# Kernel optimization log

Measured on AMD Instinct MI355X. Metric: run time of the kernel, lower is better.

Reference implementation:

```python
import jax, jax.numpy as jnp
import numpy as np

N = 50000
E = 800000
H = 96
NUM_IN = 11
PE_DIM = 24
NUM_OUT = 1
NUM_LAYERS = 4
NUM_GRAPHS = 256


def _linear_params(key, d_in, d_out):
    k1, k2 = jax.random.split(key)
    bound = 1.0 / np.sqrt(d_in)
    w = jax.random.uniform(k1, (d_in, d_out), jnp.float32, -bound, bound)
    b = jax.random.uniform(k2, (d_out,), jnp.float32, -bound, bound)
    return w, b


def setup_inputs() -> dict:
    key = jax.random.key(0)
    ks = jax.random.split(key, 32)
    x = jax.random.normal(ks[0], (N, NUM_IN), jnp.float32)
    pos = jax.random.normal(ks[1], (N, 3), jnp.float32)
    pe = jax.random.normal(ks[2], (N, PE_DIM), jnp.float32)
    edge_index = jax.random.randint(ks[3], (2, E), 0, N, jnp.int64)
    batch = jnp.sort(jax.random.randint(ks[4], (N,), 0, NUM_GRAPHS, jnp.int64))
    embed_w1, embed_b1 = _linear_params(ks[5], NUM_IN + PE_DIM, H)
    embed_w2, embed_b2 = _linear_params(ks[6], H, H)
    # per-layer stacked params
    msg_w1 = []; msg_b1 = []; msg_w2 = []; msg_b2 = []
    upd_w1 = []; upd_b1 = []; upd_w2 = []; upd_b2 = []
    for l in range(NUM_LAYERS):
        w, b = _linear_params(ks[7 + l], 2 * H + 1, H); msg_w1.append(w); msg_b1.append(b)
        w, b = _linear_params(ks[11 + l], H, H); msg_w2.append(w); msg_b2.append(b)
        w, b = _linear_params(ks[15 + l], 2 * H, H); upd_w1.append(w); upd_b1.append(b)
        w, b = _linear_params(ks[19 + l], H, H); upd_w2.append(w); upd_b2.append(b)
    pre_w1, pre_b1 = _linear_params(ks[23], H, H)
    pre_w2, pre_b2 = _linear_params(ks[24], H, H)
    ro_w1, ro_b1 = _linear_params(ks[25], H, H)
    ro_w2, ro_b2 = _linear_params(ks[26], H, NUM_OUT)
    return {
        'x': x, 'pos': pos, 'pe': pe, 'edge_index': edge_index, 'batch': batch,
        'embed_w1': embed_w1, 'embed_b1': embed_b1, 'embed_w2': embed_w2, 'embed_b2': embed_b2,
        'msg_w1': jnp.stack(msg_w1), 'msg_b1': jnp.stack(msg_b1),
        'msg_w2': jnp.stack(msg_w2), 'msg_b2': jnp.stack(msg_b2),
        'upd_w1': jnp.stack(upd_w1), 'upd_b1': jnp.stack(upd_b1),
        'upd_w2': jnp.stack(upd_w2), 'upd_b2': jnp.stack(upd_b2),
        'pre_w1': pre_w1, 'pre_b1': pre_b1, 'pre_w2': pre_w2, 'pre_b2': pre_b2,
        'ro_w1': ro_w1, 'ro_b1': ro_b1, 'ro_w2': ro_w2, 'ro_b2': ro_b2,
    }


def _egnn_forward(x, pos, pe, edge_index, batch,
                  embed_w1, embed_b1, embed_w2, embed_b2,
                  msg_w1, msg_b1, msg_w2, msg_b2,
                  upd_w1, upd_b1, upd_w2, upd_b2,
                  pre_w1, pre_b1, pre_w2, pre_b2,
                  ro_w1, ro_b1, ro_w2, ro_b2):
    silu = jax.nn.silu
    send, rec = edge_index[0], edge_index[1]
    h = jnp.concatenate([x, pe], axis=-1)
    h = silu(h @ embed_w1 + embed_b1) @ embed_w2 + embed_b2  # [N,H]
    dist = jnp.linalg.norm(pos[send] - pos[rec], axis=1)[:, None]  # [E,1]
    for l in range(NUM_LAYERS):
        state = jnp.concatenate([h[send], h[rec], dist], axis=1)  # [E,2H+1]
        msg = silu(silu(state @ msg_w1[l] + msg_b1[l]) @ msg_w2[l] + msg_b2[l])  # [E,H]
        aggr = jax.ops.segment_sum(msg, rec, num_segments=h.shape[0])  # [N,H]
        upd_in = jnp.concatenate([h, aggr], axis=1)
        update = silu(upd_in @ upd_w1[l] + upd_b1[l]) @ upd_w2[l] + upd_b2[l]
        h = h + update
    h = silu(h @ pre_w1 + pre_b1) @ pre_w2 + pre_b2
    pooled = jax.ops.segment_sum(h, batch, num_segments=NUM_GRAPHS)  # [G,H]
    out = silu(pooled @ ro_w1 + ro_b1) @ ro_w2 + ro_b2  # [G,1]
    return jnp.squeeze(out)


def reference(x, pos, pe, edge_index, batch,
              embed_w1, embed_b1, embed_w2, embed_b2,
              msg_w1, msg_b1, msg_w2, msg_b2,
              upd_w1, upd_b1, upd_w2, upd_b2,
              pre_w1, pre_b1, pre_w2, pre_b2,
              ro_w1, ro_b1, ro_w2, ro_b2):
    return _egnn_forward(x, pos, pe, edge_index, batch,
                         embed_w1, embed_b1, embed_w2, embed_b2,
                         msg_w1, msg_b1, msg_w2, msg_b2,
                         upd_w1, upd_b1, upd_w2, upd_b2,
                         pre_w1, pre_b1, pre_w2, pre_b2,
                         ro_w1, ro_b1, ro_w2, ro_b2)
```

## Files before the change

### kernel.cpp

```cpp
#include <hip/hip_runtime.h>
#include <hip/hip_bf16.h>

#define HDIM 96
#define TILE 128
#define NTILE 64

typedef __attribute__((ext_vector_type(8))) short  short8;
typedef __attribute__((ext_vector_type(4))) short  short4v;
typedef __attribute__((ext_vector_type(4))) float  float4v;
typedef __attribute__((ext_vector_type(2))) float  float2v;
typedef __attribute__((ext_vector_type(4))) unsigned int uint4v;
typedef __attribute__((ext_vector_type(2))) unsigned int uint2v;

static __device__ __forceinline__ short f2bf(float f){
    unsigned u = __float_as_uint(f);
    return (short)((u + 0x8000u) >> 16);
}
static __device__ __forceinline__ float bf2f(short s){
    unsigned u = ((unsigned)(unsigned short)s) << 16;
    return __uint_as_float(u);
}
static __device__ __forceinline__ float silu_f(float v){
    return v * __builtin_amdgcn_rcpf(1.0f + __expf(-v));
}
static __device__ __forceinline__ unsigned silu2_pack(float2v v){
    float e0 = __expf(-v[0]);
    float e1 = __expf(-v[1]);
    float2v ep = {e0, e1};
    const float2v one2 = {1.0f, 1.0f};
    ep += one2;
    float2v q = { __builtin_amdgcn_rcpf(ep[0]), __builtin_amdgcn_rcpf(ep[1]) };
    float2v res = v * q;
    unsigned pa = __float_as_uint(res[0]) + 0x8000u;
    unsigned pb = __float_as_uint(res[1]) + 0x8000u;
    return __builtin_amdgcn_perm(pb, pa, 0x07060302);
}

struct SwJob { const float* src; int ck; int ks; int ksrc; };
struct SwTable { SwJob j[22]; };

__global__ __launch_bounds__(256) void swizzle_all(SwTable T, const float* __restrict__ msg_w1,
                                                   short* __restrict__ dst, short* __restrict__ dst2,
                                                   int total1, int total2){
    int gid = blockIdx.x*256 + threadIdx.x;
    if (gid < total1) {
        int ksg = gid / 3072;
        int e   = gid % 3072;
        const float* src = T.j[0].src; int k0 = 0, ksrc = 0;
        #pragma unroll
        for (int jj = 0; jj < 22; ++jj){
            int s = T.j[jj].ck;
            if (ksg >= s && ksg < s + T.j[jj].ks){ src = T.j[jj].src; k0 = (ksg - s)*32; ksrc = T.j[jj].ksrc; }
        }
        int nt   = e >> 9;
        int rem  = e & 511;
        int lane = rem >> 3;
        int jx   = rem & 7;
        int k = k0 + ((lane >> 4) << 3) + jx;
        int f = nt*16 + (lane & 15);
        float v = (k < ksrc) ? src[(size_t)k*HDIM + f] : 0.0f;
        dst[gid] = f2bf(v);
    } else if (gid < total1 + total2) {
        int g2 = gid - total1;
        int layer = g2 / 18432;
        int e     = g2 % 18432;
        int ksg = e / 6144;
        int rem = e % 6144;
        int nt   = rem >> 9;
        int r2   = rem & 511;
        int lane = r2 >> 3;
        int jx   = r2 & 7;
        int k = ksg*32 + ((lane >> 4) << 3) + jx;
        int f = nt*16 + (lane & 15);
        int row = (f < 96) ? k : (96 + k);
        int col = (f < 96) ? f : (f - 96);
        dst2[g2] = f2bf(msg_w1[(size_t)layer*193*96 + (size_t)row*96 + col]);
    }
}

__global__ __launch_bounds__(256) void hist_kernel(const int* __restrict__ rec, int* __restrict__ deg, int E){
    int e = blockIdx.x*256 + threadIdx.x;
    if (e < E) atomicAdd(&deg[rec[e]], 1);
}

__global__ __launch_bounds__(256) void scan_part(const int* __restrict__ deg, int* __restrict__ part, int N){
    __shared__ int red[256];
    const int t = threadIdx.x;
    int base = blockIdx.x*1024;
    int s = 0;
    #pragma unroll
    for (int j=0;j<4;j++){ int i = base + j*256 + t; s += (i<N)?deg[i]:0; }
    red[t]=s; __syncthreads();
    #pragma unroll
    for (int off=128; off>0; off>>=1){ if (t<off) red[t]+=red[t+off]; __syncthreads(); }
    if (t==0) part[blockIdx.x]=red[0];
}
__global__ __launch_bounds__(256) void scan_top(int* __restrict__ part, int nb){
    __shared__ int buf[256];
    const int t = threadIdx.x;
    int v = (t < nb) ? part[t] : 0;
    buf[t] = v;
    __syncthreads();
    #pragma unroll
    for (int off=1; off<256; off<<=1){
        int u = (t>=off)?buf[t-off]:0;
        __syncthreads();
        buf[t] += u;
        __syncthreads();
    }
    if (t < nb) part[t] = buf[t] - v;
}
__global__ __launch_bounds__(256) void scan_final(const int* __restrict__ deg, const int* __restrict__ part,
                                                  int* __restrict__ cur, int N){
    __shared__ int tsum[256];
    const int t = threadIdx.x;
    int i0 = blockIdx.x*1024 + t*4;
    int a0 = (i0+0<N)?deg[i0+0]:0;
    int a1 = (i0+1<N)?deg[i0+1]:0;
    int a2 = (i0+2<N)?deg[i0+2]:0;
    int a3 = (i0+3<N)?deg[i0+3]:0;
    int s = a0+a1+a2+a3;
    tsum[t]=s; __syncthreads();
    #pragma unroll
    for (int off=1; off<256; off<<=1){
        int u = (t>=off)?tsum[t-off]:0;
        __syncthreads();
        tsum[t]+=u;
        __syncthreads();
    }
    int excl = tsum[t]-s + part[blockIdx.x];
    if (i0+0<N) cur[i0+0]=excl;
    if (i0+1<N) cur[i0+1]=excl+a0;
    if (i0+2<N) cur[i0+2]=excl+a0+a1;
    if (i0+3<N) cur[i0+3]=excl+a0+a1+a2;
}

__global__ __launch_bounds__(256) void scatter_kernel(
    const int* __restrict__ send, const int* __restrict__ rec, const float* __restrict__ pos,
    int* __restrict__ cur, int2* __restrict__ sd_s, int* __restrict__ rec_s, int E)
{
    int e = blockIdx.x*256 + threadIdx.x;
    if (e >= E) return;
    int s = send[e], r = rec[e];
    int p = atomicAdd(&cur[r], 1);
    float dx = pos[3*s]   - pos[3*r];
    float dy = pos[3*s+1] - pos[3*r+1];
    float dz = pos[3*s+2] - pos[3*r+2];
    float d = sqrtf(dx*dx + dy*dy + dz*dz);
    sd_s[p] = make_int2(s, __float_as_int(d));
    rec_s[p] = r;
}

__global__ __launch_bounds__(256,5) void edge_kernel(
    const short* __restrict__ SR,
    const int2* __restrict__ sd_s, const int* __restrict__ rec_s,
    const float* __restrict__ w1r192,
    const short* __restrict__ w2sw, const float* __restrict__ b2,
    float* __restrict__ aggr, float* __restrict__ stageA, float* __restrict__ stageB, int E)
{
    __shared__ short msgS[TILE*104];
    __shared__ int   recS[TILE];
    __shared__ int   startIdxS[TILE+1];
    __shared__ int   wcntS[2];
    const int t  = threadIdx.x;
    const int e0 = blockIdx.x * TILE;
    const int lane = t & 63;
    const int wv   = t >> 6;
    const int e_lo = wv * 32;
    const int col  = lane & 15;
    const int quad = lane >> 4;
    const int frow = quad * 4;
    const float4v fzero = {0.f,0.f,0.f,0.f};

    int se[2], re[2]; float dd[2];
    #pragma unroll
    for (int et=0; et<2; ++et){
        int ec = e0 + e_lo + et*16 + col; if (ec >= E) ec = E - 1;
        int2 sd = sd_s[ec];
        se[et] = sd.x; dd[et] = __int_as_float(sd.y);
        re[et] = rec_s[ec];
    }
    uint4v Svu[2][3], Rvu[2][3];
    #pragma unroll
    for (int et=0; et<2; ++et)
      #pragma unroll
      for (int ks=0; ks<3; ++ks){
        int f0 = ks*32 + quad*8;
        Svu[et][ks] = *(const uint4v*)(SR + (size_t)se[et]*192 + f0);
        Rvu[et][ks] = *(const uint4v*)(SR + (size_t)re[et]*192 + 96 + f0);
      }

    int myRec = 0;
    bool flag = false;
    if (t < TILE) {
        int e = e0 + t; if (e >= E) e = E - 1;
        myRec = rec_s[e];
        recS[t] = myRec;
        int ep = e0 + t - 1; if (ep >= E) ep = E - 1;
        flag = (t == 0) || (myRec != rec_s[ep]);
    }
    unsigned long long bmask = __ballot(flag ? 1 : 0);
    int pre = __popcll(bmask & ((1ull << (t & 63)) - 1ull));
    if (t < TILE && (t & 63) == 0) wcntS[t >> 6] = __popcll(bmask);

    const bool firstB = (e0 > 0) && (rec_s[e0-1] == rec_s[e0]);
    const bool lastB  = (e0 + TILE < E) && (rec_s[e0 + TILE] == rec_s[(e0+TILE-1 < E)? e0+TILE-1 : E-1]);

    __syncthreads();

    if (flag) startIdxS[pre + ((t >> 6) ? wcntS[0] : 0)] = t;
    if (t == 0) startIdxS[wcntS[0] + wcntS[1]] = TILE;

    short8 frag[2][3];
    #pragma unroll
    for (int et=0; et<2; ++et){
        float2v d2 = {dd[et], dd[et]};
        #pragma unroll
        for (int ks=0; ks<3; ++ks){
            int f0 = ks*32 + quad*8;
            float4v wa = *(const float4v*)(w1r192 + f0);
            float4v wb = *(const float4v*)(w1r192 + f0 + 4);
            uint4v su = Svu[et][ks], ru = Rvu[et][ks];
            uint4v fo;
            #pragma unroll
            for (int p=0;p<4;p++){
                float2v w2;
                if      (p==0) w2 = (float2v){wa[0], wa[1]};
                else if (p==1) w2 = (float2v){wa[2], wa[3]};
                else if (p==2) w2 = (float2v){wb[0], wb[1]};
                else           w2 = (float2v){wb[2], wb[3]};
                unsigned us = su[p], ur = ru[p];
                float2v s2 = { __uint_as_float(us << 16), __uint_as_float(us & 0xffff0000u) };
                float2v r2 = { __uint_as_float(ur << 16), __uint_as_float(ur & 0xffff0000u) };
                float2v v = s2 + r2 + d2*w2;
                fo[p] = silu2_pack(v);
            }
            short8 fr;
            __builtin_memcpy(&fr, &fo, 16);
            frag[et][ks] = fr;
        }
    }

    float4v acc2[2][6];
    #pragma unroll
    for (int i=0;i<2;i++)
      #pragma unroll
      for (int n=0;n<6;n++) acc2[i][n] = fzero;

    const short8* w2f = (const short8*)w2sw;
    #pragma unroll
    for (int ks = 0; ks < 3; ++ks) {
        #pragma unroll
        for (int mt = 0; mt < 6; ++mt) {
            short8 a = w2f[(ks*6+mt)*64 + lane];
            acc2[0][mt] = __builtin_amdgcn_mfma_f32_16x16x32_bf16(a, frag[0][ks], acc2[0][mt], 0, 0, 0);
            acc2[1][mt] = __builtin_amdgcn_mfma_f32_16x16x32_bf16(a, frag[1][ks], acc2[1][mt], 0, 0, 0);
        }
    }
    float4v b2v[6];
    #pragma unroll
    for (int mt=0; mt<6; ++mt) b2v[mt] = *(const float4v*)(b2 + mt*16 + frow);

    #pragma unroll
    for (int et=0; et<2; ++et){
        int e = e_lo + et*16 + col;
        bool valid = (e0 + e) < E;
        #pragma unroll
        for (int mt=0; mt<6; ++mt){
            float2v vlo = { acc2[et][mt][0] + b2v[mt][0], acc2[et][mt][1] + b2v[mt][1] };
            float2v vhi = { acc2[et][mt][2] + b2v[mt][2], acc2[et][mt][3] + b2v[mt][3] };
            unsigned ulo = silu2_pack(vlo);
            unsigned uhi = silu2_pack(vhi);
            if (!valid){ ulo = 0u; uhi = 0u; }
            uint2v st = {ulo, uhi};
            *(uint2v*)(msgS + e*104 + mt*16 + frow) = st;
        }
    }
    __syncthreads();

    const int nseg = wcntS[0] + wcntS[1];
    const int items = nseg * 12;
    for (int item = t; item < items; item += 256){
        int s  = item / 12;
        int fg = item - s*12;
        int r0 = startIdxS[s], r1 = startIdxS[s+1];
        float2v s01 = {0.f,0.f}, s23 = {0.f,0.f}, s45 = {0.f,0.f}, s67 = {0.f,0.f};
        for (int r = r0; r < r1; ++r){
            const unsigned* pp = (const unsigned*)(msgS + r*104 + fg*8);
            unsigned p0 = pp[0], p1 = pp[1], p2 = pp[2], p3 = pp[3];
            float2v a0 = { __uint_as_float(p0 << 16), __uint_as_float(p0 & 0xffff0000u) };
            float2v a1 = { __uint_as_float(p1 << 16), __uint_as_float(p1 & 0xffff0000u) };
            float2v a2 = { __uint_as_float(p2 << 16), __uint_as_float(p2 & 0xffff0000u) };
            float2v a3 = { __uint_as_float(p3 << 16), __uint_as_float(p3 & 0xffff0000u) };
            s01 += a0; s23 += a1; s45 += a2; s67 += a3;
        }
        int node = recS[r0];
        float* dstp;
        if (s == 0 && firstB)            dstp = stageB + (size_t)node*HDIM + fg*8;
        else if (s == nseg-1 && lastB)   dstp = stageA + (size_t)node*HDIM + fg*8;
        else                             dstp = aggr   + (size_t)node*HDIM + fg*8;
        float4v lo = {s01[0], s01[1], s23[0], s23[1]};
        float4v hi = {s45[0], s45[1], s67[0], s67[1]};
        *(float4v*)(dstp)     = lo;
        *(float4v*)(dstp + 4) = hi;
    }
}

__global__ __launch_bounds__(256,3) void update_kernel(
    short* __restrict__ hbf, const float* __restrict__ aggr,
    const float* __restrict__ stageA, const float* __restrict__ stageB,
    const int* __restrict__ deg, const int* __restrict__ cur,
    const short* __restrict__ w1sw, const float* __restrict__ b1,
    const short* __restrict__ w2sw, const float* __restrict__ b2,
    const short* __restrict__ w1sr_next, const float* __restrict__ msgb1_next,
    short* __restrict__ SR,
    const short* __restrict__ pw1, const float* __restrict__ pb1,
    const short* __restrict__ pw2, const float* __restrict__ pb2,
    const int* __restrict__ batch, float* __restrict__ pooled, int N)
{
    __shared__ short stateS[NTILE*208];
    __shared__ int   batchS[NTILE];
    __shared__ int   startIdxS[NTILE+1];
    __shared__ int   nsegS;
    const int t  = threadIdx.x;
    const int n0 = blockIdx.x * NTILE;

    #pragma unroll
    for (int it = 0; it < 6; ++it) {
        int q = it*256 + t;
        int c = q % 24;
        int i = q / 24;
        int node = n0 + i;
        if (c < 12) {
            uint4v v = {0u,0u,0u,0u};
            if (node < N) v = *(const uint4v*)(hbf + (size_t)node*HDIM + c*8);
            *(uint4v*)(stateS + i*200 + c*8) = v;
        } else {
            int cc = c - 12;
            short8 s8 = {0,0,0,0,0,0,0,0};
            if (node < N) {
                int dg = deg[node];
                int en = cur[node];
                int st = en - dg;
                bool bnd = (dg > 0) && (st/TILE != (en-1)/TILE);
                float4v a0, a1;
                if (bnd) {
                    size_t b = (size_t)node*HDIM + cc*8;
                    a0 = *(const float4v*)(stageA + b)     + *(const float4v*)(stageB + b);
                    a1 = *(const float4v*)(stageA + b + 4) + *(const float4v*)(stageB + b + 4);
                } else {
                    a0 = *(const float4v*)(aggr + (size_t)node*HDIM + cc*8);
                    a1 = *(const float4v*)(aggr + (size_t)node*HDIM + cc*8 + 4);
                }
                s8[0]=f2bf(a0[0]); s8[1]=f2bf(a0[1]); s8[2]=f2bf(a0[2]); s8[3]=f2bf(a0[3]);
                s8[4]=f2bf(a1[0]); s8[5]=f2bf(a1[1]); s8[6]=f2bf(a1[2]); s8[7]=f2bf(a1[3]);
            }
            *(short8*)(stateS + i*200 + HDIM + cc*8) = s8;
        }
    }
    __syncthreads();

    const int lane = t & 63;
    const int wv   = t >> 6;
    const int rb   = wv * 16;
    const int col  = lane & 15;
    const int quad = lane >> 4;
    const int koff = quad * 8;
    const int frow = quad * 4;
    const float4v fzero = {0.f,0.f,0.f,0.f};

    float4v acc[6];
    #pragma unroll
    for (int n=0;n<6;n++) acc[n] = fzero;

    const short8* w1f = (const short8*)w1sw;
    #pragma unroll
    for (int ks = 0; ks < 6; ++ks) {
        short8 bb = *(const short8*)(stateS + (rb+col)*200 + ks*32 + koff);
        #pragma unroll
        for (int mt = 0; mt < 6; ++mt) {
            short8 a = w1f[(ks*6+mt)*64 + lane];
            acc[mt] = __builtin_amdgcn_mfma_f32_16x16x32_bf16(a, bb, acc[mt], 0, 0, 0);
        }
    }
    float4v b1v[6];
    #pragma unroll
    for (int mt=0; mt<6; ++mt) b1v[mt] = *(const float4v*)(b1 + mt*16 + frow);
    __syncthreads();

    short* t1S = stateS;
    {
        int e = rb + col;
        #pragma unroll
        for (int mt=0; mt<6; ++mt){
            short4v sv;
            #pragma unroll
            for (int r=0;r<4;r++) sv[r] = f2bf(silu_f(acc[mt][r] + b1v[mt][r]));
            *(short4v*)(t1S + e*104 + mt*16 + frow) = sv;
        }
    }
    __syncthreads();

    float4v acc2[6];
    #pragma unroll
    for (int n=0;n<6;n++) acc2[n] = fzero;

    const short8* w2f = (const short8*)w2sw;
    #pragma unroll
    for (int ks = 0; ks < 3; ++ks) {
        short8 bb = *(const short8*)(t1S + (rb+col)*104 + ks*32 + koff);
        #pragma unroll
        for (int mt = 0; mt < 6; ++mt) {
            short8 a = w2f[(ks*6+mt)*64 + lane];
            acc2[mt] = __builtin_amdgcn_mfma_f32_16x16x32_bf16(a, bb, acc2[mt], 0, 0, 0);
        }
    }
    float4v b2v[6];
    #pragma unroll
    for (int mt=0; mt<6; ++mt) b2v[mt] = *(const float4v*)(b2 + mt*16 + frow);
    __syncthreads();

    {
        int erow = rb + col;
        int node = n0 + erow;
        bool valid = node < N;
        size_t base = (size_t)node*HDIM;
        #pragma unroll
        for (int mt=0; mt<6; ++mt){
            int f0 = mt*16 + frow;
            short4v ov = {0,0,0,0};
            if (valid) ov = *(const short4v*)(hbf + base + f0);
            float4v o;
            #pragma unroll
            for (int r=0;r<4;r++) o[r] = bf2f(ov[r]) + acc2[mt][r] + b2v[mt][r];
            short4v sv = {f2bf(o[0]), f2bf(o[1]), f2bf(o[2]), f2bf(o[3])};
            if (valid) *(short4v*)(hbf + base + f0) = sv;
            *(short4v*)(stateS + erow*104 + f0) = sv;
        }
    }

    if (w1sr_next) {
        __syncthreads();
        float4v accS[12];
        #pragma unroll
        for (int n=0;n<12;n++) accS[n] = fzero;

        const short8* wsf = (const short8*)w1sr_next;
        #pragma unroll
        for (int ks = 0; ks < 3; ++ks) {
            short8 bb = *(const short8*)(stateS + (rb+col)*104 + ks*32 + koff);
            #pragma unroll
            for (int mt = 0; mt < 12; ++mt) {
                short8 a = wsf[(ks*12+mt)*64 + lane];
                accS[mt] = __builtin_amdgcn_mfma_f32_16x16x32_bf16(a, bb, accS[mt], 0, 0, 0);
            }
        }
        float4v bnv[6];
        #pragma unroll
        for (int mt=0; mt<6; ++mt) bnv[mt] = *(const float4v*)(msgb1_next + mt*16 + frow);

        {
            int node = n0 + rb + col;
            if (node < N) {
                size_t sbase = (size_t)node*192;
                #pragma unroll
                for (int mt=0; mt<12; ++mt){
                    float4v o = accS[mt];
                    if (mt < 6) { o[0]+=bnv[mt][0]; o[1]+=bnv[mt][1]; o[2]+=bnv[mt][2]; o[3]+=bnv[mt][3]; }
                    short4v sv = {f2bf(o[0]), f2bf(o[1]), f2bf(o[2]), f2bf(o[3])};
                    *(short4v*)(SR + sbase + mt*16 + frow) = sv;
                }
            }
        }
    } else if (pw1) {
        if (t < NTILE) {
            int node = n0 + t;
            batchS[t] = batch[node < N ? node : N-1];
        }
        __syncthreads();

        bool flag = false;
        if (t < NTILE) flag = (t == 0) || (batchS[t] != batchS[t-1]);
        unsigned long long bm = __ballot(flag ? 1 : 0);
        if (t < NTILE) {
            int pre = __popcll(bm & ((1ull << t) - 1ull));
            if (flag) startIdxS[pre] = t;
            if (t == 0) nsegS = __popcll(bm);
        }

        float4v accp[6];
        #pragma unroll
        for (int n=0;n<6;n++) accp[n] = fzero;

        const short8* pw1f = (const short8*)pw1;
        #pragma unroll
        for (int ks = 0; ks < 3; ++ks) {
            short8 bb = *(const short8*)(stateS + (rb+col)*104 + ks*32 + koff);
            #pragma unroll
            for (int mt = 0; mt < 6; ++mt) {
                short8 a = pw1f[(ks*6+mt)*64 + lane];
                accp[mt] = __builtin_amdgcn_mfma_f32_16x16x32_bf16(a, bb, accp[mt], 0, 0, 0);
            }
        }
        float4v pb1v[6];
        #pragma unroll
        for (int mt=0; mt<6; ++mt) pb1v[mt] = *(const float4v*)(pb1 + mt*16 + frow);

        short* t1p = stateS + NTILE*104;
        {
            int e = rb + col;
            #pragma unroll
            for (int mt=0; mt<6; ++mt){
                short4v sv;
                #pragma unroll
                for (int r=0;r<4;r++) sv[r] = f2bf(silu_f(accp[mt][r] + pb1v[mt][r]));
                *(short4v*)(t1p + e*104 + mt*16 + frow) = sv;
            }
        }
        __syncthreads();

        float4v accq[6];
        #pragma unroll
        for (int n=0;n<6;n++) accq[n] = fzero;

        const short8* pw2f = (const short8*)pw2;
        #pragma unroll
        for (int ks = 0; ks < 3; ++ks) {
            short8 bb = *(const short8*)(t1p + (rb+col)*104 + ks*32 + koff);
            #pragma unroll
            for (int mt = 0; mt < 6; ++mt) {
                short8 a = pw2f[(ks*6+mt)*64 + lane];
                accq[mt] = __builtin_amdgcn_mfma_f32_16x16x32_bf16(a, bb, accq[mt], 0, 0, 0);
            }
        }
        float4v pb2v[6];
        #pragma unroll
        for (int mt=0; mt<6; ++mt) pb2v[mt] = *(const float4v*)(pb2 + mt*16 + frow);
        __syncthreads();

        float* msgS = (float*)stateS;
        {
            int e = rb + col;
            bool valid = (n0 + e) < N;
            #pragma unroll
            for (int mt=0; mt<6; ++mt){
                float4v v;
                #pragma unroll
                for (int r=0;r<4;r++){
                    float u = accq[mt][r] + pb2v[mt][r];
                    v[r] = valid ? u : 0.0f;
                }
                *(float4v*)(msgS + e*100 + mt*16 + frow) = v;
            }
        }
        __syncthreads();

        const int nseg = nsegS;
        if (t == 0) startIdxS[nseg] = NTILE;
        __syncthreads();

        const int items = nseg * 24;
        for (int item = t; item < items; item += 256){
            int s  = item / 24;
            int fg = item - s*24;
            int r0 = startIdxS[s], r1 = startIdxS[s+1];
            float4v sum = fzero;
            for (int r = r0; r < r1; ++r) sum += *(const float4v*)(msgS + r*100 + fg*4);
            float* dstp = pooled + (size_t)batchS[r0]*HDIM + fg*4;
            atomicAdd(dstp+0, sum[0]);
            atomicAdd(dstp+1, sum[1]);
            atomicAdd(dstp+2, sum[2]);
            atomicAdd(dstp+3, sum[3]);
        }
    }
}

__global__ __launch_bounds__(256,3) void embed_kernel(
    const float* __restrict__ x, const float* __restrict__ pe,
    const short* __restrict__ w1sw, const float* __restrict__ b1,
    const short* __restrict__ w2sw, const float* __restrict__ b2,
    short* __restrict__ hbf,
    const short* __restrict__ w1sr0, const float* __restrict__ msgb1_0,
    short* __restrict__ SR, int N)
{
    __shared__ short stateS[NTILE*72];
    __shared__ short t1S[NTILE*104];
    const int t  = threadIdx.x;
    const int n0 = blockIdx.x * NTILE;

    if (t < NTILE) {
        int node = n0 + t;
        short* row = stateS + t*72;
        if (node < N) {
            #pragma unroll
            for (int j=0;j<11;j++) row[j]    = f2bf(x[(size_t)node*11 + j]);
            #pragma unroll
            for (int j=0;j<24;j++) row[11+j] = f2bf(pe[(size_t)node*24 + j]);
            #pragma unroll
            for (int j=35;j<64;j++) row[j] = 0;
        } else {
            #pragma unroll
            for (int j=0;j<64;j++) row[j] = 0;
        }
    }
    __syncthreads();

    const int lane = t & 63;
    const int wv   = t >> 6;
    const int rb   = wv * 16;
    const int col  = lane & 15;
    const int quad = lane >> 4;
    const int koff = quad * 8;
    const int frow = quad * 4;
    const float4v fzero = {0.f,0.f,0.f,0.f};

    float4v acc[6];
    #pragma unroll
    for (int n=0;n<6;n++) acc[n] = fzero;

    const short8* w1f = (const short8*)w1sw;
    #pragma unroll
    for (int ks = 0; ks < 2; ++ks) {
        short8 bb = *(const short8*)(stateS + (rb+col)*72 + ks*32 + koff);
        #pragma unroll
        for (int mt = 0; mt < 6; ++mt) {
            short8 a = w1f[(ks*6+mt)*64 + lane];
            acc[mt] = __builtin_amdgcn_mfma_f32_16x16x32_bf16(a, bb, acc[mt], 0, 0, 0);
        }
    }
    float4v b1v[6];
    #pragma unroll
    for (int mt=0; mt<6; ++mt) b1v[mt] = *(const float4v*)(b1 + mt*16 + frow);

    {
        int e = rb + col;
        #pragma unroll
        for (int mt=0; mt<6; ++mt){
            short4v sv;
            #pragma unroll
            for (int r=0;r<4;r++) sv[r] = f2bf(silu_f(acc[mt][r] + b1v[mt][r]));
            *(short4v*)(t1S + e*104 + mt*16 + frow) = sv;
        }
    }
    __syncthreads();

    float4v acc2[6];
    #pragma unroll
    for (int n=0;n<6;n++) acc2[n] = fzero;

    const short8* w2f = (const short8*)w2sw;
    #pragma unroll
    for (int ks = 0; ks < 3; ++ks) {
        short8 bb = *(const short8*)(t1S + (rb+col)*104 + ks*32 + koff);
        #pragma unroll
        for (int mt = 0; mt < 6; ++mt) {
            short8 a = w2f[(ks*6+mt)*64 + lane];
            acc2[mt] = __builtin_amdgcn_mfma_f32_16x16x32_bf16(a, bb, acc2[mt], 0, 0, 0);
        }
    }
    float4v b2v[6];
    #pragma unroll
    for (int mt=0; mt<6; ++mt) b2v[mt] = *(const float4v*)(b2 + mt*16 + frow);
    __syncthreads();

    {
        int erow = rb + col;
        int node = n0 + erow;
        bool valid = node < N;
        size_t base = (size_t)node*HDIM;
        #pragma unroll
        for (int mt=0; mt<6; ++mt){
            int f0 = mt*16 + frow;
            float4v o;
            #pragma unroll
            for (int r=0;r<4;r++) o[r] = acc2[mt][r] + b2v[mt][r];
            short4v sv = {f2bf(o[0]), f2bf(o[1]), f2bf(o[2]), f2bf(o[3])};
            if (valid) *(short4v*)(hbf + base + f0) = sv;
            *(short4v*)(t1S + erow*104 + f0) = sv;
        }
    }
    __syncthreads();

    float4v accS[12];
    #pragma unroll
    for (int n=0;n<12;n++) accS[n] = fzero;

    const short8* wsf = (const short8*)w1sr0;
    #pragma unroll
    for (int ks = 0; ks < 3; ++ks) {
        short8 bb = *(const short8*)(t1S + (rb+col)*104 + ks*32 + koff);
        #pragma unroll
        for (int mt = 0; mt < 12; ++mt) {
            short8 a = wsf[(ks*12+mt)*64 + lane];
            accS[mt] = __builtin_amdgcn_mfma_f32_16x16x32_bf16(a, bb, accS[mt], 0, 0, 0);
        }
    }
    float4v bnv[6];
    #pragma unroll
    for (int mt=0; mt<6; ++mt) bnv[mt] = *(const float4v*)(msgb1_0 + mt*16 + frow);

    {
        int node = n0 + rb + col;
        if (node < N) {
            size_t sbase = (size_t)node*192;
            #pragma unroll
            for (int mt=0; mt<12; ++mt){
                float4v o = accS[mt];
                if (mt < 6) { o[0]+=bnv[mt][0]; o[1]+=bnv[mt][1]; o[2]+=bnv[mt][2]; o[3]+=bnv[mt][3]; }
                short4v sv = {f2bf(o[0]), f2bf(o[1]), f2bf(o[2]), f2bf(o[3])};
                *(short4v*)(SR + sbase + mt*16 + frow) = sv;
            }
        }
    }
}

__global__ __launch_bounds__(128) void readout_kernel(
    const float* __restrict__ pooled,
    const float* __restrict__ w1, const float* __restrict__ b1,
    const float* __restrict__ w2, const float* __restrict__ b2,
    float* __restrict__ out)
{
    __shared__ float red[128];
    const int g = blockIdx.x;
    const int t = threadIdx.x;
    float p = 0.0f;
    if (t < HDIM) {
        float acc = b1[t];
        for (int k = 0; k < HDIM; ++k)
            acc += pooled[(size_t)g*HDIM + k] * w1[(size_t)k*HDIM + t];
        acc = silu_f(acc);
        p = acc * w2[t];
    }
    red[t] = p;
    __syncthreads();
    for (int s = 64; s > 0; s >>= 1) {
        if (t < s) red[t] += red[t + s];
        __syncthreads();
    }
    if (t == 0) out[g] = red[0] + b2[0];
}

extern "C" void kernel_launch(void* const* d_in, const int* in_sizes, int n_in,
                              void* d_out, int out_size, void* d_ws, size_t ws_size,
                              hipStream_t stream)
{
    const float* x        = (const float*)d_in[0];
    const float* pos      = (const float*)d_in[1];
    const float* pe       = (const float*)d_in[2];
    const int*   ei       = (const int*)d_in[3];
    const int*   batch    = (const int*)d_in[4];
    const float* embed_w1 = (const float*)d_in[5];
    const float* embed_b1 = (const float*)d_in[6];
    const float* embed_w2 = (const float*)d_in[7];
    const float* embed_b2 = (const float*)d_in[8];
    const float* msg_w1   = (const float*)d_in[9];
    const float* msg_b1   = (const float*)d_in[10];
    const float* msg_w2   = (const float*)d_in[11];
    const float* msg_b2   = (const float*)d_in[12];
    const float* upd_w1   = (const float*)d_in[13];
    const float* upd_b1   = (const float*)d_in[14];
    const float* upd_w2   = (const float*)d_in[15];
    const float* upd_b2   = (const float*)d_in[16];
    const float* pre_w1   = (const float*)d_in[17];
    const float* pre_b1   = (const float*)d_in[18];
    const float* pre_w2   = (const float*)d_in[19];
    const float* pre_b2   = (const float*)d_in[20];
    const float* ro_w1    = (const float*)d_in[21];
    const float* ro_b1    = (const float*)d_in[22];
    const float* ro_w2    = (const float*)d_in[23];
    const float* ro_b2    = (const float*)d_in[24];

    const int E = in_sizes[3] / 2;
    const int N = in_sizes[4];
    const int G = out_size;

    char* ws = (char*)d_ws;
    size_t off = 0;
    auto alloc = [&](size_t bytes){ void* p = ws + off; off += (bytes + 255) & ~(size_t)255; return p; };
    short* hbf    = (short*)alloc((size_t)N*HDIM*2);
    float* aggr   = (float*)alloc((size_t)N*HDIM*4);
    float* stageA = (float*)alloc((size_t)N*HDIM*4);
    float* stageB = (float*)alloc((size_t)N*HDIM*4);
    float* pooled = (float*)alloc((size_t)G*HDIM*4);
    short* wsw    = (short*)alloc((size_t)59*3072*2);
    short* w1sr   = (short*)alloc((size_t)4*18432*2);
    short* SR     = (short*)alloc((size_t)N*192*2);
    int*   deg    = (int*)alloc((size_t)N*4);
    int*   cur    = (int*)alloc((size_t)N*4);
    int*   part   = (int*)alloc((size_t)256*4);
    int2*  sd_s   = (int2*)alloc((size_t)E*8);
    int*   rec_s  = (int*)alloc((size_t)E*4);

    hipMemsetAsync(aggr,   0, (size_t)N*HDIM*4, stream);
    hipMemsetAsync(pooled, 0, (size_t)G*HDIM*4, stream);
    hipMemsetAsync(deg,    0, (size_t)N*4, stream);

    SwTable T;
    for (int jj=0;jj<22;jj++){ T.j[jj].src = embed_w1; T.j[jj].ck = 1<<30; T.j[jj].ks = 0; T.j[jj].ksrc = 0; }
    int ck = 0, ji = 0;
    auto add = [&](const float* s, int ks, int ksrc){
        T.j[ji].src = s; T.j[ji].ck = ck; T.j[ji].ks = ks; T.j[ji].ksrc = ksrc;
        ji++; ck += ks;
    };
    add(embed_w1, 2, 35);
    add(embed_w2, 3, 96);
    add(pre_w1,   3, 96);
    add(pre_w2,   3, 96);
    for (int l=0;l<4;l++) add(msg_w2 + (size_t)l*96*96,  3, 96);
    for (int l=0;l<4;l++) add(upd_w1 + (size_t)l*192*96, 6, 192);
    for (int l=0;l<4;l++) add(upd_w2 + (size_t)l*96*96,  3, 96);
    const int total1 = 59*3072;
    const int total2 = 4*18432;
    swizzle_all<<<(total1+total2+255)/256, 256, 0, stream>>>(T, msg_w1, wsw, w1sr, total1, total2);

    const int nbE256 = (E + 255) / 256;
    const int nbScan = (N + 1023) / 1024;
    hist_kernel<<<nbE256, 256, 0, stream>>>(ei + E, deg, E);
    scan_part<<<nbScan, 256, 0, stream>>>(deg, part, N);
    scan_top<<<1, 256, 0, stream>>>(part, nbScan);
    scan_final<<<nbScan, 256, 0, stream>>>(deg, part, cur, N);
    scatter_kernel<<<nbE256, 256, 0, stream>>>(ei, ei + E, pos, cur, sd_s, rec_s, E);

    const int nbN = (N + NTILE - 1) / NTILE;
    embed_kernel<<<nbN, 256, 0, stream>>>(x, pe, wsw + 0, embed_b1, wsw + 2*3072, embed_b2,
                                          hbf, w1sr, msg_b1, SR, N);

    const int nbE = (E + TILE - 1) / TILE;
    for (int l = 0; l < 4; ++l) {
        edge_kernel<<<nbE, 256, 0, stream>>>(SR, sd_s, rec_s,
            msg_w1 + (size_t)l*193*96 + (size_t)192*96,
            wsw + (11 + 3*l)*3072, msg_b2 + l*96, aggr, stageA, stageB, E);
        const short* w1sr_next  = (l < 3) ? (w1sr + (size_t)(l+1)*18432) : nullptr;
        const float* msgb1_next = (l < 3) ? (msg_b1 + (l+1)*96) : nullptr;
        const short* pw1 = (l == 3) ? (wsw + 5*3072) : nullptr;
        const float* pb1 = (l == 3) ? pre_b1 : nullptr;
        const short* pw2 = (l == 3) ? (wsw + 8*3072) : nullptr;
        const float* pb2 = (l == 3) ? pre_b2 : nullptr;
        update_kernel<<<nbN, 256, 0, stream>>>(hbf, aggr, stageA, stageB, deg, cur,
            wsw + (23 + 6*l)*3072, upd_b1 + l*96,
            wsw + (47 + 3*l)*3072, upd_b2 + l*96,
            w1sr_next, msgb1_next, SR,
            pw1, pb1, pw2, pb2, batch, pooled, N);
    }

    readout_kernel<<<G, 128, 0, stream>>>(pooled, ro_w1, ro_b1, ro_w2, ro_b2, (float*)d_out);
}
```

Before: 736.4 us.

## Stage sender-row gathers into LDS via async global_load_lds and widen segment reduction

```diff
diff --git a/kernel.cpp b/kernel.cpp
--- a/kernel.cpp
+++ b/kernel.cpp
@@ -34,6 +34,12 @@
     unsigned pa = __float_as_uint(res[0]) + 0x8000u;
     unsigned pb = __float_as_uint(res[1]) + 0x8000u;
     return __builtin_amdgcn_perm(pb, pa, 0x07060302);
+}
+
+typedef __attribute__((address_space(1))) const unsigned int guint;
+typedef __attribute__((address_space(3))) unsigned int luint;
+static __device__ __forceinline__ void gload_lds16(const void* g, void* l){
+    __builtin_amdgcn_global_load_lds((guint*)g, (luint*)l, 16, 0, 0);
 }
 
 struct SwJob { const float* src; int ck; int ks; int ksrc; };
@@ -172,21 +178,42 @@
     const int frow = quad * 4;
     const float4v fzero = {0.f,0.f,0.f,0.f};
 
-    int se[2], re[2]; float dd[2];
+    int seStage[7], ccStage[7];
+    #pragma unroll
+    for (int i=0;i<7;i++){
+        int idx = i*4 + wv;
+        if (idx < 26){
+            int s  = idx*64 + lane;
+            int es = s/13;
+            int cc = s - es*13; if (cc > 11) cc = 11;
+            int ec = e0 + es; if (ec >= E) ec = E - 1;
+            seStage[i] = ((const int*)sd_s)[2*ec];
+            ccStage[i] = cc;
+        }
+    }
+    #pragma unroll
+    for (int i=0;i<7;i++){
+        int idx = i*4 + wv;
+        if (idx < 26){
+            const short* src = SR + (size_t)seStage[i]*192 + ccStage[i]*8;
+            gload_lds16(src, msgS + idx*512);
+        }
+    }
+
+    int re[2]; float dd[2];
     #pragma unroll
     for (int et=0; et<2; ++et){
         int ec = e0 + e_lo + et*16 + col; if (ec >= E) ec = E - 1;
         int2 sd = sd_s[ec];
-        se[et] = sd.x; dd[et] = __int_as_float(sd.y);
+        dd[et] = __int_as_float(sd.y);
         re[et] = rec_s[ec];
     }
-    uint4v Svu[2][3], Rvu[2][3];
+    uint4v Rvu[2][3];
     #pragma unroll
     for (int et=0; et<2; ++et)
       #pragma unroll
       for (int ks=0; ks<3; ++ks){
         int f0 = ks*32 + quad*8;
-        Svu[et][ks] = *(const uint4v*)(SR + (size_t)se[et]*192 + f0);
         Rvu[et][ks] = *(const uint4v*)(SR + (size_t)re[et]*192 + 96 + f0);
       }
 
@@ -215,12 +242,14 @@
     #pragma unroll
     for (int et=0; et<2; ++et){
         float2v d2 = {dd[et], dd[et]};
+        int e_local = e_lo + et*16 + col;
         #pragma unroll
         for (int ks=0; ks<3; ++ks){
             int f0 = ks*32 + quad*8;
             float4v wa = *(const float4v*)(w1r192 + f0);
             float4v wb = *(const float4v*)(w1r192 + f0 + 4);
-            uint4v su = Svu[et][ks], ru = Rvu[et][ks];
+            uint4v su = *(const uint4v*)(msgS + e_local*104 + (ks*4+quad)*8);
+            uint4v ru = Rvu[et][ks];
             uint4v fo;
             #pragma unroll
             for (int p=0;p<4;p++){
@@ -240,6 +269,7 @@
             frag[et][ks] = fr;
         }
     }
+    __syncthreads();
 
     float4v acc2[2][6];
     #pragma unroll
@@ -279,30 +309,26 @@
     __syncthreads();
 
     const int nseg = wcntS[0] + wcntS[1];
-    const int items = nseg * 12;
+    const int items = nseg * 24;
     for (int item = t; item < items; item += 256){
-        int s  = item / 12;
-        int fg = item - s*12;
+        int s  = item / 24;
+        int fg = item - s*24;
         int r0 = startIdxS[s], r1 = startIdxS[s+1];
-        float2v s01 = {0.f,0.f}, s23 = {0.f,0.f}, s45 = {0.f,0.f}, s67 = {0.f,0.f};
+        float2v s01 = {0.f,0.f}, s23 = {0.f,0.f};
         for (int r = r0; r < r1; ++r){
-            const unsigned* pp = (const unsigned*)(msgS + r*104 + fg*8);
-            unsigned p0 = pp[0], p1 = pp[1], p2 = pp[2], p3 = pp[3];
+            const unsigned* pp = (const unsigned*)(msgS + r*104 + fg*4);
+            unsigned p0 = pp[0], p1 = pp[1];
             float2v a0 = { __uint_as_float(p0 << 16), __uint_as_float(p0 & 0xffff0000u) };
             float2v a1 = { __uint_as_float(p1 << 16), __uint_as_float(p1 & 0xffff0000u) };
-            float2v a2 = { __uint_as_float(p2 << 16), __uint_as_float(p2 & 0xffff0000u) };
-            float2v a3 = { __uint_as_float(p3 << 16), __uint_as_float(p3 & 0xffff0000u) };
-            s01 += a0; s23 += a1; s45 += a2; s67 += a3;
+            s01 += a0; s23 += a1;
         }
         int node = recS[r0];
         float* dstp;
-        if (s == 0 && firstB)            dstp = stageB + (size_t)node*HDIM + fg*8;
-        else if (s == nseg-1 && lastB)   dstp = stageA + (size_t)node*HDIM + fg*8;
-        else                             dstp = aggr   + (size_t)node*HDIM + fg*8;
-        float4v lo = {s01[0], s01[1], s23[0], s23[1]};
-        float4v hi = {s45[0], s45[1], s67[0], s67[1]};
-        *(float4v*)(dstp)     = lo;
-        *(float4v*)(dstp + 4) = hi;
+        if (s == 0 && firstB)            dstp = stageB + (size_t)node*HDIM + fg*4;
+        else if (s == nseg-1 && lastB)   dstp = stageA + (size_t)node*HDIM + fg*4;
+        else                             dstp = aggr   + (size_t)node*HDIM + fg*4;
+        float4v v = {s01[0], s01[1], s23[0], s23[1]};
+        *(float4v*)(dstp) = v;
     }
 }
 
```

Result: faster. 716.7 us (-2.7%).
